# Kernel optimization log

Hardware: AMD Instinct MI355X
Metric: run time of the kernel (lower is better)

The kernel has to match this reference:

```python
import jax, jax.numpy as jnp
import numpy as np

HEADS = 32
KV_HEADS = 8
HEAD_DIM = 128
ROPE_THETA = 10000.0


def _rope_tables(position_ids, head_dim, dtype):
    # position_ids: [S] int
    inv_freq = 1.0 / (ROPE_THETA ** (jnp.arange(0, head_dim, 2, dtype=jnp.float32) / head_dim))
    freqs = position_ids.astype(jnp.float32)[:, None] * inv_freq[None, :]   # [S, hd/2]
    emb = jnp.concatenate([freqs, freqs], axis=-1)                          # [S, hd]
    return jnp.cos(emb).astype(dtype), jnp.sin(emb).astype(dtype)


def _rotate_half(x):
    h = x.shape[-1] // 2
    return jnp.concatenate([-x[..., h:], x[..., :h]], axis=-1)


def setup_inputs() -> dict:
    key = jax.random.key(0)
    ks = jax.random.split(key, 5)
    B, S, D = 2, 2048, 4096
    kv_dim = KV_HEADS * HEAD_DIM
    s = 0.02
    return {
        "hidden_states": jax.random.normal(ks[0], (B, S, D), jnp.float32),
        "position_ids": jnp.arange(S, dtype=jnp.int64 if jax.config.jax_enable_x64 else jnp.int32),
        "wq": jax.random.normal(ks[1], (D, D), jnp.float32) * s,
        "wk": jax.random.normal(ks[2], (kv_dim, D), jnp.float32) * s,
        "wv": jax.random.normal(ks[3], (kv_dim, D), jnp.float32) * s,
        "wo": jax.random.normal(ks[4], (D, D), jnp.float32) * s,
    }


def reference(hidden_states, position_ids, wq, wk, wv, wo):
    B, S, D = hidden_states.shape
    groups = HEADS // KV_HEADS

    # Q/K/V projections (nn.Linear: x @ W.T), split into heads -> [B, H, S, hd]
    q = (hidden_states @ wq.T).reshape(B, S, HEADS, HEAD_DIM).transpose(0, 2, 1, 3)
    k = (hidden_states @ wk.T).reshape(B, S, KV_HEADS, HEAD_DIM).transpose(0, 2, 1, 3)
    v = (hidden_states @ wv.T).reshape(B, S, KV_HEADS, HEAD_DIM).transpose(0, 2, 1, 3)

    # RoPE
    cos, sin = _rope_tables(position_ids, HEAD_DIM, q.dtype)  # [S, hd]
    q = q * cos + _rotate_half(q) * sin
    k = k * cos + _rotate_half(k) * sin

    # GQA: expand KV heads to match Q heads
    k = jnp.repeat(k, groups, axis=1)  # [B, H, S, hd]
    v = jnp.repeat(v, groups, axis=1)

    # causal SDPA
    scale = 1.0 / jnp.sqrt(jnp.asarray(HEAD_DIM, q.dtype))
    scores = jnp.einsum("bhqd,bhkd->bhqk", q, k) * scale
    causal = jnp.tril(jnp.ones((S, S), dtype=bool))
    scores = jnp.where(causal, scores, jnp.finfo(scores.dtype).min)
    probs = jax.nn.softmax(scores, axis=-1)
    attn = jnp.einsum("bhqk,bhkd->bhqd", probs, v)  # [B, H, S, hd]

    # merge heads + output projection
    attn = attn.transpose(0, 2, 1, 3).reshape(B, S, D)
    return attn @ wo.T
```

## Files before the change

### kernel.cpp

```cpp
#include <hip/hip_runtime.h>
#include <hip/hip_bf16.h>
#include <math.h>

typedef __attribute__((ext_vector_type(8))) short short8;
typedef __attribute__((ext_vector_type(4))) float f32x4;
typedef __attribute__((ext_vector_type(16))) float f32x16;
typedef __attribute__((ext_vector_type(4))) unsigned int u32x4;
typedef __attribute__((ext_vector_type(2))) int i32x2;

#define BATCH   2
#define SLEN    2048
#define DMODEL  4096
#define NHEADS  32
#define KVHEADS 8
#define HD      128
#define KVDIM   (KVHEADS*HD)
#define MROWS   (BATCH*SLEN)
#define NQKV    (DMODEL + 2*KVDIM)

#define GLDS16(gp, lp) __builtin_amdgcn_global_load_lds( \
    (const __attribute__((address_space(1))) void*)(gp), \
    (__attribute__((address_space(3))) void*)(lp), 16, 0, 0)

static __device__ __forceinline__ unsigned short bf16bits(float x) {
    __hip_bfloat16 h = __float2bfloat16(x);
    return *(unsigned short*)&h;
}
static __device__ __forceinline__ float bf2f(unsigned short u) {
    __hip_bfloat16 h = *(__hip_bfloat16*)&u;
    return __bfloat162float(h);
}
static __device__ __forceinline__ unsigned cvtpk(float a, float b) {
    unsigned r;
    asm("v_cvt_pk_bf16_f32 %0, %1, %2" : "=v"(r) : "v"(a), "v"(b));
    return r;
}

__global__ __launch_bounds__(256) void cast_k(const float* __restrict__ in,
                                              unsigned short* __restrict__ out, long n) {
    long i = ((long)blockIdx.x * 256 + threadIdx.x) * 4;
    if (i >= n) return;
    float4 v = *(const float4*)(in + i);
    union { unsigned short h[4]; uint2 u; } c;
    c.h[0] = bf16bits(v.x); c.h[1] = bf16bits(v.y);
    c.h[2] = bf16bits(v.z); c.h[3] = bf16bits(v.w);
    *(uint2*)(out + i) = c.u;
}

__global__ void rope_table_k(const int* __restrict__ pos,
                             float* __restrict__ cosT, float* __restrict__ sinT) {
    int s = blockIdx.x;
    int d = threadIdx.x;
    float p = (float)pos[s];
    float inv = powf(10000.0f, -(float)(2 * d) / 128.0f);
    float ang = p * inv;
    cosT[s * 64 + d] = cosf(ang);
    sinT[s * 64 + d] = sinf(ang);
}

__global__ void rope_bf_k(unsigned short* __restrict__ x,
                          const float* __restrict__ cosT, const float* __restrict__ sinT,
                          int nh, int ld, float mul) {
    int idx = blockIdx.x * 256 + threadIdx.x;
    int d = idx & 63;
    int rest = idx >> 6;
    int h = rest % nh;
    int row = rest / nh;
    int s = row & (SLEN - 1);
    float c  = cosT[s * 64 + d] * mul;
    float sn = sinT[s * 64 + d] * mul;
    unsigned short* base = x + (size_t)row * ld + h * HD;
    float x1 = bf2f(base[d]), x2 = bf2f(base[d + 64]);
    base[d]      = bf16bits(x1 * c - x2 * sn);
    base[d + 64] = bf16bits(x2 * c + x1 * sn);
}

__global__ __launch_bounds__(256) void vtrans_k(const unsigned short* __restrict__ V, int ldv,
                                                unsigned short* __restrict__ Vt) {
    __shared__ unsigned short L[64][144];
    const int t = threadIdx.x;
    const int s0 = blockIdx.x * 64;
    const int bk = blockIdx.y;
    const int b = bk >> 3, kvh = bk & 7;
    #pragma unroll
    for (int j = 0; j < 4; ++j) {
        int idx = t + j * 256;
        int row = idx >> 4;
        int c8  = (idx & 15) * 8;
        *(short8*)&L[row][c8] =
            *(const short8*)(V + ((size_t)b * SLEN + s0 + row) * ldv + kvh * HD + c8);
    }
    __syncthreads();
    {
        int d  = t >> 1;
        int sh = (t & 1) * 32;
        unsigned short tmp[32];
        #pragma unroll
        for (int j = 0; j < 32; ++j) tmp[j] = L[sh + j][d];
        unsigned short* dst = Vt + ((size_t)bk * HD + d) * SLEN + s0 + sh;
        #pragma unroll
        for (int j = 0; j < 4; ++j)
            *(short8*)(dst + j * 8) = *(const short8*)(tmp + j * 8);
    }
}

template<typename CT>
__global__ __launch_bounds__(512, 1) void gemm256(
    const unsigned short* __restrict__ A, int lda,
    const unsigned short* __restrict__ W, int ldw,
    CT* __restrict__ C, int ldc,
    int M, int N, int K)
{
    __shared__ unsigned short Asl[2][2][128 * 64];
    __shared__ unsigned short Bsl[2][2][128 * 64];

    const int t = threadIdx.x;
    const int w = t >> 6, lane = t & 63;

    const int gx = gridDim.x;
    const int nwg = gx * gridDim.y;
    const int chunk = nwg >> 3;
    const int orig = blockIdx.y * gx + blockIdx.x;
    const int xcd = orig & 7, idx = orig >> 3;
    const int rn = chunk >> 3;
    const int nrx = gx / rn;
    const int rx = xcd % nrx, ry = xcd / nrx;
    const int iy = idx / rn, ix = idx % rn;
    const int m0 = (ry * 8 + iy) * 256;
    const int n0 = (rx * rn + ix) * 256;

    const int wm = (w >> 2) * 128;
    const int wn = (w & 3) * 64;
    const int fr = lane & 15, hi = lane >> 4;

    f32x4 acc[8][4];
    #pragma unroll
    for (int i = 0; i < 8; ++i)
        #pragma unroll
        for (int j = 0; j < 4; ++j)
            acc[i][j] = (f32x4){0.f, 0.f, 0.f, 0.f};

    const int sr = t >> 3;
    const int sl = t & 7;
    const int wv512 = w * 512;

    {
        #pragma unroll
        for (int hh = 0; hh < 4; ++hh) {
            #pragma unroll
            for (int j = 0; j < 2; ++j) {
                const int row = j * 64 + sr;
                const int scol = (sl ^ (row & 7)) << 3;
                if (hh < 2)
                    GLDS16(W + (size_t)(n0 + hh * 128 + row) * ldw + scol,
                           &Bsl[0][hh][j * 4096 + wv512]);
                else
                    GLDS16(A + (size_t)(m0 + (hh - 2) * 128 + row) * lda + scol,
                           &Asl[0][hh - 2][j * 4096 + wv512]);
            }
        }
        asm volatile("s_waitcnt vmcnt(0)" ::: "memory");
        __builtin_amdgcn_s_barrier();
        __builtin_amdgcn_sched_barrier(0);
    }

    const int NT = K >> 6;
    int buf = 0;
    for (int kt = 0; kt < NT; ++kt) {
        const unsigned short* Ah = Asl[buf][w >> 2];
        const unsigned short* Bh = Bsl[buf][(w & 3) >> 1];
        const bool pf = (kt + 1 < NT);
        const int k0n = (kt + 1) << 6;
        short8 bfr[4][2];

        #pragma unroll
        for (int q = 0; q < 4; ++q) {
            if (q == 0) {
                #pragma unroll
                for (int j = 0; j < 4; ++j) {
                    const int lr = (wn & 127) + j * 16 + fr;
                    const int sz = lr & 7;
                    bfr[j][0] = *(const short8*)&Bh[lr * 64 + (((0 + hi) ^ sz) << 3)];
                    bfr[j][1] = *(const short8*)&Bh[lr * 64 + (((4 + hi) ^ sz) << 3)];
                }
            }
            short8 af[2][2];
            #pragma unroll
            for (int ii = 0; ii < 2; ++ii) {
                const int lr = q * 32 + ii * 16 + fr;
                const int sz = lr & 7;
                af[ii][0] = *(const short8*)&Ah[lr * 64 + (((0 + hi) ^ sz) << 3)];
                af[ii][1] = *(const short8*)&Ah[lr * 64 + (((4 + hi) ^ sz) << 3)];
            }

            if (pf) {
                if (q < 2) {
                    #pragma unroll
                    for (int j = 0; j < 2; ++j) {
                        const int row = j * 64 + sr;
                        const int scol = k0n + ((sl ^ (row & 7)) << 3);
                        GLDS16(W + (size_t)(n0 + q * 128 + row) * ldw + scol,
                               &Bsl[buf ^ 1][q][j * 4096 + wv512]);
                    }
                } else if (q == 2) {
                    #pragma unroll
                    for (int half = 0; half < 2; ++half)
                        #pragma unroll
                        for (int j = 0; j < 2; ++j) {
                            const int row = j * 64 + sr;
                            const int scol = k0n + ((sl ^ (row & 7)) << 3);
                            GLDS16(A + (size_t)(m0 + half * 128 + row) * lda + scol,
                                   &Asl[buf ^ 1][half][j * 4096 + wv512]);
                        }
                }
            }

            __builtin_amdgcn_sched_barrier(0);
            __builtin_amdgcn_s_barrier();
            __builtin_amdgcn_sched_barrier(0);

            __builtin_amdgcn_s_setprio(1);
            #pragma unroll
            for (int ii = 0; ii < 2; ++ii)
                #pragma unroll
                for (int j = 0; j < 4; ++j) {
                    acc[q * 2 + ii][j] = __builtin_amdgcn_mfma_f32_16x16x32_bf16(
                        af[ii][0], bfr[j][0], acc[q * 2 + ii][j], 0, 0, 0);
                    acc[q * 2 + ii][j] = __builtin_amdgcn_mfma_f32_16x16x32_bf16(
                        af[ii][1], bfr[j][1], acc[q * 2 + ii][j], 0, 0, 0);
                }
            __builtin_amdgcn_s_setprio(0);

            if (q == 3 && pf)
                asm volatile("s_waitcnt vmcnt(0)" ::: "memory");

            __builtin_amdgcn_sched_barrier(0);
            __builtin_amdgcn_s_barrier();
            __builtin_amdgcn_sched_barrier(0);
        }
        buf ^= 1;
    }

    const int crow = (lane >> 4) * 4, ccol = lane & 15;
    #pragma unroll
    for (int i = 0; i < 8; ++i)
        #pragma unroll
        for (int j = 0; j < 4; ++j) {
            CT* cp = C + (size_t)(m0 + wm + i * 16 + crow) * ldc + (n0 + wn + j * 16 + ccol);
            #pragma unroll
            for (int r = 0; r < 4; ++r) {
                if constexpr (sizeof(CT) == 2)
                    cp[(size_t)r * ldc] = bf16bits(acc[i][j][r]);
                else
                    cp[(size_t)r * ldc] = acc[i][j][r];
            }
        }
}

__global__ __launch_bounds__(256, 2) void flash_mfma32(
    const unsigned short* __restrict__ Qb, int ldq,
    const unsigned short* __restrict__ Kb, int ldk,
    const unsigned short* __restrict__ Vt,
    unsigned short* __restrict__ Ob)
{
    __shared__ unsigned short Ks[2][64 * 128];
    __shared__ unsigned short Vs[2][128 * 64];

    const int t = threadIdx.x;
    const int wid = t >> 6, lane = t & 63;
    const int qt = (int)gridDim.x - 1 - (int)blockIdx.x;
    const int bh = blockIdx.y;
    const int b = bh >> 5, h = bh & 31, kvh = h >> 2;
    const int lq = lane & 31;
    const int hl = lane >> 5;
    const int qw0 = qt * 128 + wid * 32;
    const int qg = qw0 + lq;
    const size_t qrowg = (size_t)b * SLEN + qg;

    const unsigned short* Kg0 = Kb + (size_t)b * SLEN * ldk + kvh * HD;
    const unsigned short* Vg0 = Vt + (size_t)(b * KVHEADS + kvh) * HD * SLEN;

    auto STAGE = [&](int buf, int kt) {
        const unsigned short* Kg = Kg0 + (size_t)kt * 64 * ldk;
        #pragma unroll
        for (int i = 0; i < 4; ++i) {
            int row = i * 16 + (t >> 4);
            int colel = ((((t & 15) << 4) ^ ((row & 15) << 4)) >> 1);
            GLDS16(Kg + (size_t)row * ldk + colel, &Ks[buf][i * 2048 + wid * 512]);
        }
        const unsigned short* Vg = Vg0 + kt * 64;
        #pragma unroll
        for (int i = 0; i < 4; ++i) {
            int row = i * 32 + (t >> 3);
            int colel = ((((t & 7) << 4) ^ ((row & 7) << 4)) >> 1);
            GLDS16(Vg + (size_t)row * SLEN + colel, &Vs[buf][i * 2048 + wid * 512]);
        }
    };

    STAGE(0, 0);
    short8 qf[8];
    {
        const unsigned short* qp = Qb + qrowg * ldq + h * HD + hl * 8;
        #pragma unroll
        for (int dt = 0; dt < 8; ++dt)
            qf[dt] = *(const short8*)(qp + dt * 16);
    }

    f32x16 accO[4];
    #pragma unroll
    for (int db = 0; db < 4; ++db)
        #pragma unroll
        for (int r = 0; r < 16; ++r) accO[db][r] = 0.f;
    float m_i = -INFINITY, l_i = 0.f;

    const int ntmax = 2 * qt + 2;
    int p = 0;
    for (int kt = 0; kt < ntmax; ++kt) {
        if (kt + 1 < ntmax) {
            STAGE(p ^ 1, kt + 1);
            asm volatile("s_waitcnt vmcnt(8)" ::: "memory");
        } else {
            asm volatile("s_waitcnt vmcnt(0)" ::: "memory");
        }
        __builtin_amdgcn_s_barrier();
        __builtin_amdgcn_sched_barrier(0);

        const unsigned short* Kp = Ks[p];
        const unsigned short* Vp = Vs[p];

        f32x16 sc[2];
        #pragma unroll
        for (int blk = 0; blk < 2; ++blk) {
            #pragma unroll
            for (int r = 0; r < 16; ++r) sc[blk][r] = 0.f;
            __builtin_amdgcn_s_setprio(1);
            #pragma unroll
            for (int dt = 0; dt < 8; ++dt) {
                int krow = blk * 32 + lq;
                int kb = krow * 256 + ((dt * 32 + hl * 16) ^ ((krow & 15) << 4));
                short8 kf = *(const short8*)(Kp + (kb >> 1));
                sc[blk] = __builtin_amdgcn_mfma_f32_32x32x16_bf16(kf, qf[dt], sc[blk], 0, 0, 0);
            }
            __builtin_amdgcn_s_setprio(0);
        }

        if (kt * 64 + 63 > qw0) {
            #pragma unroll
            for (int blk = 0; blk < 2; ++blk)
                #pragma unroll
                for (int r = 0; r < 16; ++r) {
                    int kv = kt * 64 + blk * 32 + (r & 3) + 8 * (r >> 2) + 4 * hl;
                    if (kv > qg) sc[blk][r] = -INFINITY;
                }
        }

        float pmax = sc[0][0];
        #pragma unroll
        for (int r = 1; r < 16; ++r) pmax = fmaxf(pmax, sc[0][r]);
        #pragma unroll
        for (int r = 0; r < 16; ++r) pmax = fmaxf(pmax, sc[1][r]);
        {
            i32x2 mr = __builtin_amdgcn_permlane32_swap(__float_as_int(pmax), __float_as_int(pmax), false, false);
            pmax = fmaxf(__int_as_float(mr.x), __int_as_float(mr.y));
        }

        if (!__all(pmax <= m_i + 8.0f)) {
            float mn = fmaxf(m_i, pmax);
            float al = exp2f(m_i - mn);
            m_i = mn;
            l_i *= al;
            #pragma unroll
            for (int db = 0; db < 4; ++db)
                #pragma unroll
                for (int r = 0; r < 16; ++r) accO[db][r] *= al;
        }

        float rs = 0.f;
        #pragma unroll
        for (int blk = 0; blk < 2; ++blk)
            #pragma unroll
            for (int r = 0; r < 16; ++r) {
                float pv = exp2f(sc[blk][r] - m_i);
                sc[blk][r] = pv;
                rs += pv;
            }
        {
            i32x2 sr = __builtin_amdgcn_permlane32_swap(__float_as_int(rs), __float_as_int(rs), false, false);
            rs = __int_as_float(sr.x) + __int_as_float(sr.y);
        }
        l_i += rs;

        short8 pf[4];
        #pragma unroll
        for (int blk = 0; blk < 2; ++blk) {
            unsigned c01 = cvtpk(sc[blk][0],  sc[blk][1]);
            unsigned c23 = cvtpk(sc[blk][2],  sc[blk][3]);
            unsigned c45 = cvtpk(sc[blk][4],  sc[blk][5]);
            unsigned c67 = cvtpk(sc[blk][6],  sc[blk][7]);
            i32x2 sA = __builtin_amdgcn_permlane32_swap((int)c01, (int)c45, false, false);
            i32x2 sB = __builtin_amdgcn_permlane32_swap((int)c23, (int)c67, false, false);
            u32x4 f0 = {(unsigned)sA.x, (unsigned)sB.x, (unsigned)sA.y, (unsigned)sB.y};
            pf[blk * 2] = *(short8*)&f0;
            unsigned c89 = cvtpk(sc[blk][8],  sc[blk][9]);
            unsigned cab = cvtpk(sc[blk][10], sc[blk][11]);
            unsigned ccd = cvtpk(sc[blk][12], sc[blk][13]);
            unsigned cef = cvtpk(sc[blk][14], sc[blk][15]);
            i32x2 sC = __builtin_amdgcn_permlane32_swap((int)c89, (int)ccd, false, false);
            i32x2 sD = __builtin_amdgcn_permlane32_swap((int)cab, (int)cef, false, false);
            u32x4 f1 = {(unsigned)sC.x, (unsigned)sD.x, (unsigned)sC.y, (unsigned)sD.y};
            pf[blk * 2 + 1] = *(short8*)&f1;
        }

        #pragma unroll
        for (int db = 0; db < 4; ++db) {
            __builtin_amdgcn_s_setprio(1);
            #pragma unroll
            for (int ks = 0; ks < 4; ++ks) {
                int vrow = db * 32 + lq;
                int vb = vrow * 128 + ((ks * 32 + hl * 16) ^ ((vrow & 7) << 4));
                short8 vf = *(const short8*)(Vp + (vb >> 1));
                accO[db] = __builtin_amdgcn_mfma_f32_32x32x16_bf16(vf, pf[ks], accO[db], 0, 0, 0);
            }
            __builtin_amdgcn_s_setprio(0);
        }

        __builtin_amdgcn_sched_barrier(0);
        __builtin_amdgcn_s_barrier();
        p ^= 1;
    }

    float inv = 1.0f / l_i;
    unsigned short* orow = Ob + qrowg * DMODEL + h * HD;
    #pragma unroll
    for (int db = 0; db < 4; ++db)
        #pragma unroll
        for (int rq = 0; rq < 4; ++rq) {
            unsigned w0 = cvtpk(accO[db][rq * 4 + 0] * inv, accO[db][rq * 4 + 1] * inv);
            unsigned w1 = cvtpk(accO[db][rq * 4 + 2] * inv, accO[db][rq * 4 + 3] * inv);
            uint2 pkd; pkd.x = w0; pkd.y = w1;
            *(uint2*)(orow + db * 32 + rq * 8 + hl * 4) = pkd;
        }
}

extern "C" void kernel_launch(void* const* d_in, const int* in_sizes, int n_in,
                              void* d_out, int out_size, void* d_ws, size_t ws_size,
                              hipStream_t stream) {
    const float* hs  = (const float*)d_in[0];
    const int*   pos = (const int*)d_in[1];
    const float* wq  = (const float*)d_in[2];
    const float* wk  = (const float*)d_in[3];
    const float* wv  = (const float*)d_in[4];
    const float* wo  = (const float*)d_in[5];
    float* out = (float*)d_out;

    char* ws = (char*)d_ws;
    unsigned short* hs_bf   = (unsigned short*)(ws);
    unsigned short* wqkv_bf = (unsigned short*)(ws + ((size_t)32  << 20));
    unsigned short* wo_bf   = (unsigned short*)(ws + ((size_t)80  << 20));
    unsigned short* qkv_bf  = (unsigned short*)(ws + ((size_t)112 << 20));
    unsigned short* Vtb     = (unsigned short*)(ws + ((size_t)160 << 20));
    unsigned short* Obf     = (unsigned short*)(ws + ((size_t)168 << 20));
    float*          cosT    = (float*)(ws + ((size_t)200 << 20));
    float*          sinT    = (float*)(ws + ((size_t)200 << 20) + (size_t)SLEN * 64 * 4);

    const long nHS = (long)MROWS * DMODEL;
    const long nWQ = (long)DMODEL * DMODEL;
    const long nWK = (long)KVDIM * DMODEL;

    rope_table_k<<<SLEN, 64, 0, stream>>>(pos, cosT, sinT);

    cast_k<<<nHS / 4 / 256, 256, 0, stream>>>(hs, hs_bf, nHS);
    cast_k<<<nWQ / 4 / 256, 256, 0, stream>>>(wq, wqkv_bf, nWQ);
    cast_k<<<nWK / 4 / 256, 256, 0, stream>>>(wk, wqkv_bf + (size_t)DMODEL * DMODEL, nWK);
    cast_k<<<nWK / 4 / 256, 256, 0, stream>>>(wv, wqkv_bf + (size_t)(DMODEL + KVDIM) * DMODEL, nWK);
    cast_k<<<nWQ / 4 / 256, 256, 0, stream>>>(wo, wo_bf, nWQ);

    gemm256<unsigned short><<<dim3(NQKV/256, MROWS/256), 512, 0, stream>>>(
        hs_bf, DMODEL, wqkv_bf, DMODEL, qkv_bf, NQKV, MROWS, NQKV, DMODEL);

    const float qmul = 0.088388347648318447f * 1.4426950408889634f;
    rope_bf_k<<<(MROWS * NHEADS  * 64) / 256, 256, 0, stream>>>(qkv_bf,          cosT, sinT, NHEADS,  NQKV, qmul);
    rope_bf_k<<<(MROWS * KVHEADS * 64) / 256, 256, 0, stream>>>(qkv_bf + DMODEL, cosT, sinT, KVHEADS, NQKV, 1.0f);
    vtrans_k<<<dim3(SLEN/64, BATCH*KVHEADS), 256, 0, stream>>>(qkv_bf + DMODEL + KVDIM, NQKV, Vtb);

    flash_mfma32<<<dim3(SLEN/128, BATCH*NHEADS), 256, 0, stream>>>(
        qkv_bf, NQKV, qkv_bf + DMODEL, NQKV, Vtb, Obf);

    gemm256<float><<<dim3(DMODEL/256, MROWS/256), 512, 0, stream>>>(
        Obf, DMODEL, wo_bf, DMODEL, out, DMODEL, MROWS, DMODEL, DMODEL);
}
```

Before: 651.1 us.

## Restage GEMM tile loads so each wave's LDS chunks wait on fine-grained vmcnt

Tile staging is reorganized so A is loaded per half by the waves that consume it, and B and A prefetches are spread evenly over the four inner sub-steps. Full vmcnt(0) drains plus two barriers per sub-step are replaced by partial vmcnt waits and one barrier placed just before each sub-step's LDS reads. The aim is to overlap global-to-LDS copies with MFMA work and halve barrier count. The risk is subtle correctness dependence on the exact count of outstanding loads and on the ordering of cross-wave LDS writes versus reads.

```diff
diff --git a/kernel.cpp b/kernel.cpp
--- a/kernel.cpp
+++ b/kernel.cpp
@@ -140,41 +140,55 @@
         for (int j = 0; j < 4; ++j)
             acc[i][j] = (f32x4){0.f, 0.f, 0.f, 0.f};
 
-    const int sr = t >> 3;
     const int sl = t & 7;
+    const int srw = (t >> 3) & 7;
     const int wv512 = w * 512;
 
-    {
-        #pragma unroll
-        for (int hh = 0; hh < 4; ++hh) {
-            #pragma unroll
-            for (int j = 0; j < 2; ++j) {
-                const int row = j * 64 + sr;
-                const int scol = (sl ^ (row & 7)) << 3;
-                if (hh < 2)
-                    GLDS16(W + (size_t)(n0 + hh * 128 + row) * ldw + scol,
-                           &Bsl[0][hh][j * 4096 + wv512]);
-                else
-                    GLDS16(A + (size_t)(m0 + (hh - 2) * 128 + row) * lda + scol,
-                           &Asl[0][hh - 2][j * 4096 + wv512]);
-            }
-        }
-        asm volatile("s_waitcnt vmcnt(0)" ::: "memory");
-        __builtin_amdgcn_s_barrier();
-        __builtin_amdgcn_sched_barrier(0);
-    }
+    auto STAGE_B = [&](int bufn, int k0, int u) {
+        const int row = u * 64 + (t >> 3);
+        const int scol = k0 + ((sl ^ srw) << 3);
+        GLDS16(W + (size_t)(n0 + row) * ldw + scol,
+               &Bsl[bufn][u >> 1][(u & 1) * 4096 + wv512]);
+    };
+    auto STAGE_A = [&](int bufn, int k0, int u) {
+        const int half = w >> 2;
+        const int row = half * 128 + u * 32 + ((t & 255) >> 3);
+        const int scol = k0 + ((sl ^ srw) << 3);
+        GLDS16(A + (size_t)(m0 + row) * lda + scol,
+               &Asl[bufn][half][u * 2048 + (w & 3) * 512]);
+    };
+
+    STAGE_B(0, 0, 0); STAGE_B(0, 0, 1); STAGE_B(0, 0, 2); STAGE_B(0, 0, 3);
+    STAGE_A(0, 0, 0); STAGE_A(0, 0, 1); STAGE_A(0, 0, 2); STAGE_A(0, 0, 3);
 
     const int NT = K >> 6;
     int buf = 0;
     for (int kt = 0; kt < NT; ++kt) {
+        const bool pf = (kt + 1 < NT);
+        const int k0n = (kt + 1) << 6;
         const unsigned short* Ah = Asl[buf][w >> 2];
         const unsigned short* Bh = Bsl[buf][(w & 3) >> 1];
-        const bool pf = (kt + 1 < NT);
-        const int k0n = (kt + 1) << 6;
         short8 bfr[4][2];
 
         #pragma unroll
         for (int q = 0; q < 4; ++q) {
+            if (q == 0) {
+                asm volatile("s_waitcnt vmcnt(3)" ::: "memory");
+                __builtin_amdgcn_s_barrier();
+            } else if (q == 1) {
+                if (pf) asm volatile("s_waitcnt vmcnt(4)" ::: "memory");
+                else    asm volatile("s_waitcnt vmcnt(2)" ::: "memory");
+                __builtin_amdgcn_s_barrier();
+            } else if (q == 2) {
+                if (pf) asm volatile("s_waitcnt vmcnt(4)" ::: "memory");
+                else    asm volatile("s_waitcnt vmcnt(1)" ::: "memory");
+                __builtin_amdgcn_s_barrier();
+            } else if (!pf) {
+                asm volatile("s_waitcnt vmcnt(0)" ::: "memory");
+                __builtin_amdgcn_s_barrier();
+            }
+            __builtin_amdgcn_sched_barrier(0);
+
             if (q == 0) {
                 #pragma unroll
                 for (int j = 0; j < 4; ++j) {
@@ -194,30 +208,11 @@
             }
 
             if (pf) {
-                if (q < 2) {
-                    #pragma unroll
-                    for (int j = 0; j < 2; ++j) {
-                        const int row = j * 64 + sr;
-                        const int scol = k0n + ((sl ^ (row & 7)) << 3);
-                        GLDS16(W + (size_t)(n0 + q * 128 + row) * ldw + scol,
-                               &Bsl[buf ^ 1][q][j * 4096 + wv512]);
-                    }
-                } else if (q == 2) {
-                    #pragma unroll
-                    for (int half = 0; half < 2; ++half)
-                        #pragma unroll
-                        for (int j = 0; j < 2; ++j) {
-                            const int row = j * 64 + sr;
-                            const int scol = k0n + ((sl ^ (row & 7)) << 3);
-                            GLDS16(A + (size_t)(m0 + half * 128 + row) * lda + scol,
-                                   &Asl[buf ^ 1][half][j * 4096 + wv512]);
-                        }
-                }
-            }
-
-            __builtin_amdgcn_sched_barrier(0);
-            __builtin_amdgcn_s_barrier();
-            __builtin_amdgcn_sched_barrier(0);
+                if (q == 0)      { STAGE_B(buf ^ 1, k0n, 0); STAGE_B(buf ^ 1, k0n, 1); }
+                else if (q == 1) { STAGE_B(buf ^ 1, k0n, 2); STAGE_B(buf ^ 1, k0n, 3); }
+                else if (q == 2) { STAGE_A(buf ^ 1, k0n, 0); STAGE_A(buf ^ 1, k0n, 1); }
+                else             { STAGE_A(buf ^ 1, k0n, 2); STAGE_A(buf ^ 1, k0n, 3); }
+            }
 
             __builtin_amdgcn_s_setprio(1);
             #pragma unroll
@@ -230,12 +225,6 @@
                         af[ii][1], bfr[j][1], acc[q * 2 + ii][j], 0, 0, 0);
                 }
             __builtin_amdgcn_s_setprio(0);
-
-            if (q == 3 && pf)
-                asm volatile("s_waitcnt vmcnt(0)" ::: "memory");
-
-            __builtin_amdgcn_sched_barrier(0);
-            __builtin_amdgcn_s_barrier();
             __builtin_amdgcn_sched_barrier(0);
         }
         buf ^= 1;
```

Result: faster. 625.4 us (-4.0%).
